# Optimization experiments

Measured on AMD Instinct MI355X. Metric: run time of the kernel, lower is better.

## Reference

```python
import jax, jax.numpy as jnp
import numpy as np

B, H, W, C = 8, 64, 64, 256  # N = H*W = 4096, pooled length N//2 = 2048


def setup_inputs() -> dict:
    key = jax.random.key(0)
    k1, k2, k3, k4 = jax.random.split(key, 4)
    scale = np.sqrt(2.0 / C).astype(np.float32)  # he_normal for 1x1 conv
    return {
        "x": jax.random.normal(k1, (B, H, W, C), dtype=jnp.float32),
        "w_theta": jax.random.normal(k2, (C, C), dtype=jnp.float32) * scale,
        "w_phi": jax.random.normal(k3, (C, C), dtype=jnp.float32) * scale,
        "w_g": jax.random.normal(k4, (C, C), dtype=jnp.float32) * scale,
    }


def _maxpool1d(z):
    # MaxPool1D(pool_size=2, strides=2, padding='valid') over axis 1
    b, n, c = z.shape
    return jnp.max(z.reshape(b, n // 2, 2, c), axis=2)


def reference(x, w_theta, w_phi, w_g):
    b, h, w, c = x.shape
    n = h * w
    xf = x.reshape(b, n, c)                       # [B, N, C]
    theta = xf @ w_theta                          # [B, N, C] (1x1 conv)
    phi = _maxpool1d(xf @ w_phi)                  # [B, N//2, C]
    f = jnp.einsum('bnc,bmc->bnm', theta, phi)    # [B, N, N//2] affinity
    f = jax.nn.softmax(f, axis=-1)
    g = _maxpool1d(xf @ w_g)                      # [B, N//2, C]
    y = jnp.einsum('bnm,bmc->bnc', f, g)          # [B, N, C]
    y = y.reshape(b, h, w, c)
    return x + y                                  # residual
```

## Files before the change

kernel.cpp:

```cpp
#include <hip/hip_runtime.h>
#include <stdint.h>

#define CC 256
#define NN 4096
#define MM 2048
#define BB 8
#define NROWS (BB*NN)
#define PROWS (BB*MM)

typedef __attribute__((ext_vector_type(8))) short    short8;
typedef __attribute__((ext_vector_type(8))) _Float16 half8;
typedef __attribute__((ext_vector_type(4))) float    float4v;

__device__ __forceinline__ unsigned short f2bf(float f) {
    unsigned int u = __float_as_uint(f);
    u += 0x7fffu + ((u >> 16) & 1u);
    return (unsigned short)(u >> 16);
}
__device__ __forceinline__ float bf2f(unsigned short h) {
    return __uint_as_float(((unsigned int)h) << 16);
}
__device__ __forceinline__ unsigned short f2h(float f) {
    union { _Float16 h; unsigned short u; } cv; cv.h = (_Float16)f; return cv.u;
}
__device__ __forceinline__ float h2f(unsigned short u) {
    union { _Float16 h; unsigned short u; } cv; cv.u = u; return (float)cv.h;
}

__global__ __launch_bounds__(256) void xsplit_kernel(
    const float* __restrict__ x,
    unsigned short* __restrict__ x_hi,
    unsigned short* __restrict__ x_lo)
{
    const size_t i = ((size_t)blockIdx.x*256 + threadIdx.x) * 8;
    float4v a0 = *(const float4v*)(x + i);
    float4v a1 = *(const float4v*)(x + i + 4);
    short8 h, l;
    #pragma unroll
    for (int j = 0; j < 4; ++j) {
        unsigned short h0 = f2bf(a0[j]);
        h[j]   = (short)h0; l[j]   = (short)f2bf(a0[j] - bf2f(h0));
        unsigned short h1 = f2bf(a1[j]);
        h[4+j] = (short)h1; l[4+j] = (short)f2bf(a1[j] - bf2f(h1));
    }
    *(short8*)(x_hi + i) = h;
    *(short8*)(x_lo + i) = l;
}

__global__ void wsplit_kernel(const float* __restrict__ w_theta,
                              const float* __restrict__ w_phi,
                              const float* __restrict__ w_g,
                              unsigned short* __restrict__ wT_hi,
                              unsigned short* __restrict__ wT_lo)
{
    __shared__ float tile[64][65];
    const int widx = blockIdx.z;
    const int kt = blockIdx.x, ct = blockIdx.y;
    const float* w = (widx == 0) ? w_theta : (widx == 1) ? w_phi : w_g;
    const int t  = threadIdx.x;
    const int tc = t & 63, tr = t >> 6;
    #pragma unroll
    for (int i = 0; i < 16; ++i) {
        const int lk = tr*16 + i;
        tile[lk][tc] = w[(size_t)(kt*64 + lk)*CC + ct*64 + tc];
    }
    __syncthreads();
    #pragma unroll
    for (int i = 0; i < 16; ++i) {
        const int lc = tr*16 + i;
        float v = tile[tc][lc];
        const int c = ct*64 + lc, k = kt*64 + tc;
        unsigned short hh = f2bf(v);
        size_t o = ((size_t)widx*CC + c)*CC + k;
        wT_hi[o] = hh;
        wT_lo[o] = f2bf(v - bf2f(hh));
    }
}

__global__ __launch_bounds__(256, 4) void proj_kernel(
    const unsigned short* __restrict__ x_hi,
    const unsigned short* __restrict__ x_lo,
    const unsigned short* __restrict__ wT_hi,
    const unsigned short* __restrict__ wT_lo,
    unsigned short* __restrict__ th,
    unsigned short* __restrict__ ph,
    unsigned short* __restrict__ g_f)
{
    __shared__ unsigned short wt_hi[64*136];
    __shared__ unsigned short wt_lo[64*136];

    const int tid  = threadIdx.x;
    const int rb   = blockIdx.x & 511;
    const int cv   = blockIdx.x >> 9;
    const int r0   = rb * 64;
    const int widx = cv >> 2;
    const int wc0  = (cv & 3) * 64;
    const unsigned short* wThp = wT_hi + ((size_t)widx*CC + wc0)*CC;
    const unsigned short* wTlp = wT_lo + ((size_t)widx*CC + wc0)*CC;
    const bool split3 = (widx < 2);

    const int wv   = tid >> 6;
    const int lane = tid & 63;
    const int quad = lane >> 4;
    const int l15  = lane & 15;
    const int arow = r0 + wv*16 + l15;
    const unsigned short* axh = x_hi + (size_t)arow*CC + quad*8;
    const unsigned short* axl = x_lo + (size_t)arow*CC + quad*8;

    float4v acc[4];
    #pragma unroll
    for (int nf = 0; nf < 4; ++nf) acc[nf] = (float4v){0.f,0.f,0.f,0.f};

    for (int h = 0; h < 2; ++h) {
        __syncthreads();
        {
            const int j    = tid & 63;
            const int kseg = tid >> 6;
            const size_t base = (size_t)j*CC + h*128 + kseg*32;
            const unsigned short* sh = wThp + base;
            unsigned short* dh = &wt_hi[j*136 + kseg*32];
            #pragma unroll
            for (int u = 0; u < 4; ++u)
                *(uint4*)(dh + u*8) = *(const uint4*)(sh + u*8);
            if (split3) {
                const unsigned short* sl = wTlp + base;
                unsigned short* dl = &wt_lo[j*136 + kseg*32];
                #pragma unroll
                for (int u = 0; u < 4; ++u)
                    *(uint4*)(dl + u*8) = *(const uint4*)(sl + u*8);
            }
        }
        __syncthreads();

        #pragma unroll
        for (int ks = 0; ks < 4; ++ks) {
            short8 a_hi = *(const short8*)(axh + h*128 + ks*32);
            short8 a_lo;
            if (split3) a_lo = *(const short8*)(axl + h*128 + ks*32);
            #pragma unroll
            for (int nf = 0; nf < 4; ++nf) {
                const int wrow = nf*16 + l15;
                short8 b_hi = *(const short8*)&wt_hi[wrow*136 + ks*32 + quad*8];
                acc[nf] = __builtin_amdgcn_mfma_f32_16x16x32_bf16(a_hi, b_hi, acc[nf], 0,0,0);
                if (split3) {
                    short8 b_lo = *(const short8*)&wt_lo[wrow*136 + ks*32 + quad*8];
                    acc[nf] = __builtin_amdgcn_mfma_f32_16x16x32_bf16(a_hi, b_lo, acc[nf], 0,0,0);
                    acc[nf] = __builtin_amdgcn_mfma_f32_16x16x32_bf16(a_lo, b_hi, acc[nf], 0,0,0);
                }
            }
        }
    }

    const int rowbase = r0 + wv*16 + quad*4;
    if (widx == 0) {
        #pragma unroll
        for (int nf = 0; nf < 4; ++nf) {
            const int c = wc0 + nf*16 + l15;
            #pragma unroll
            for (int r = 0; r < 4; ++r)
                th[(size_t)(rowbase + r)*CC + c] = f2h(acc[nf][r]);
        }
    } else if (widx == 1) {
        #pragma unroll
        for (int nf = 0; nf < 4; ++nf) {
            const int c = wc0 + nf*16 + l15;
            #pragma unroll
            for (int rp = 0; rp < 2; ++rp) {
                float v = fmaxf(acc[nf][2*rp], acc[nf][2*rp+1]);
                const int prow = rowbase/2 + rp;
                ph[(size_t)prow*CC + c] = f2h(v);
            }
        }
    } else {
        #pragma unroll
        for (int nf = 0; nf < 4; ++nf) {
            const int c = wc0 + nf*16 + l15;
            const int ct = c >> 4;
            const int c15 = c & 15;
            #pragma unroll
            for (int rp = 0; rp < 2; ++rp) {
                float v = fmaxf(acc[nf][2*rp], acc[nf][2*rp+1]);
                const int prow = rowbase/2 + rp;
                const int b  = prow >> 11;
                const int m  = prow & 2047;
                const int kt = m >> 5;
                const int km = m & 31;
                const int lane_t = (km >> 3)*16 + c15;
                const int j = km & 7;
                g_f[(((size_t)(b*64 + kt)*16 + ct)*64 + lane_t)*8 + j] = f2bf(v);
            }
        }
    }
}

__global__ void phimean_kernel(const unsigned short* __restrict__ ph,
                               float* __restrict__ phbar)
{
    const int b = blockIdx.x >> 6, chunk = blockIdx.x & 63;
    const int c = threadIdx.x;
    const size_t base = ((size_t)b*MM + chunk*32)*CC + c;
    float s = 0.f;
    for (int r = 0; r < 32; ++r) s += h2f(ph[base + (size_t)r*CC]);
    atomicAdd(&phbar[b*CC + c], s * (1.0f/MM));
}

__global__ __launch_bounds__(256, 3) void attn_kernel(
    const float* __restrict__ x,
    const unsigned short* __restrict__ th,
    const unsigned short* __restrict__ ph,
    const unsigned short* __restrict__ g_f,
    const float* __restrict__ phbar,
    float* __restrict__ out)
{
    __shared__ unsigned short s_ph[2][32*264];
    __shared__ unsigned short s_p[4][16*40];
    __shared__ float          s_l[64];

    const int tid  = threadIdx.x;
    const int bb   = blockIdx.x & 7;
    const int qt   = blockIdx.x >> 3;
    const int q0   = bb*NN + qt*64;
    const int b    = bb;
    const int wv   = tid >> 6;
    const int lane = tid & 63;
    const int quad = lane >> 4;
    const int l15  = lane & 15;

    const int sti = tid >> 3;
    const int stc = (tid & 7) * 32;
    const size_t phbase = (size_t)b * MM * CC;
    const unsigned short* stsrc = ph + phbase + (size_t)sti*CC + stc;

    half8 t_hi[8];
    {
        const unsigned short* bh = th + (size_t)(q0 + wv*16 + l15)*CC;
        #pragma unroll
        for (int ks = 0; ks < 8; ++ks)
            t_hi[ks] = *(const half8*)(bh + ks*32 + quad*8);
    }

    float sh128[4];
    {
        float sp = 0.f;
        #pragma unroll
        for (int ks = 0; ks < 8; ++ks) {
            const int k0 = ks*32 + quad*8;
            float4v m0 = *(const float4v*)&phbar[b*CC + k0];
            float4v m1 = *(const float4v*)&phbar[b*CC + k0 + 4];
            #pragma unroll
            for (int j = 0; j < 4; ++j) {
                sp += (float)t_hi[ks][j]   * m0[j];
                sp += (float)t_hi[ks][4+j] * m1[j];
            }
        }
        sp += __shfl_xor(sp, 16);
        sp += __shfl_xor(sp, 32);
        #pragma unroll
        for (int r = 0; r < 4; ++r)
            sh128[r] = __shfl(sp, quad*4 + r) + 128.f;
    }

    float4v O[4][4];
    #pragma unroll
    for (int rt = 0; rt < 4; ++rt)
        #pragma unroll
        for (int ct = 0; ct < 4; ++ct) O[rt][ct] = (float4v){0.f,0.f,0.f,0.f};
    float4v accl = (float4v){0.f,0.f,0.f,0.f};

    short8 ones;
    #pragma unroll
    for (int j = 0; j < 8; ++j) ones[j] = (short)0x3F80;

    const unsigned short* glf = g_f + (size_t)b*MM*CC + (size_t)lane*8;

    {
        unsigned short* dh = &s_ph[0][sti*264 + stc];
        #pragma unroll
        for (int u = 0; u < 4; ++u)
            *(uint4*)(dh + u*8) = *(const uint4*)(stsrc + u*8);
    }
    __syncthreads();

    for (int kt = 0; kt < 64; ++kt) {
        const int key0 = kt * 32;
        const int cur  = kt & 1;

        uint4 stg[4];
        if (kt < 63) {
            const unsigned short* sn = stsrc + (size_t)(key0 + 32)*CC;
            #pragma unroll
            for (int u = 0; u < 4; ++u) stg[u] = *(const uint4*)(sn + u*8);
        }
        short8 gf[4];
        #pragma unroll
        for (int ct = 0; ct < 4; ++ct)
            gf[ct] = *(const short8*)(glf + (size_t)(kt*16 + wv*4 + ct)*512);

        float4v S0 = (float4v){0.f,0.f,0.f,0.f};
        float4v S1 = (float4v){0.f,0.f,0.f,0.f};
        #pragma unroll
        for (int ks = 0; ks < 8; ++ks) {
            half8 b0 = *(const half8*)&s_ph[cur][( 0 + l15)*264 + ks*32 + quad*8];
            half8 b1 = *(const half8*)&s_ph[cur][(16 + l15)*264 + ks*32 + quad*8];
            S0 = __builtin_amdgcn_mfma_f32_16x16x32_f16(t_hi[ks], b0, S0, 0,0,0);
            S1 = __builtin_amdgcn_mfma_f32_16x16x32_f16(t_hi[ks], b1, S1, 0,0,0);
        }

        unsigned short* pw = &s_p[wv][0];
        #pragma unroll
        for (int r = 0; r < 4; ++r) {
            float a0 = fminf(fmaxf(S0[r] - sh128[r], -85.f), 85.f);
            float a1 = fminf(fmaxf(S1[r] - sh128[r], -85.f), 85.f);
            pw[(quad*4 + r)*40 + l15]      = f2bf(__expf(a0));
            pw[(quad*4 + r)*40 + 16 + l15] = f2bf(__expf(a1));
        }
        asm volatile("s_waitcnt lgkmcnt(0)" ::: "memory");
        short8 pown = *(const short8*)&s_p[wv][l15*40 + quad*8];
        accl = __builtin_amdgcn_mfma_f32_16x16x32_bf16(pown, ones, accl, 0,0,0);

        if (kt < 63) {
            unsigned short* dh = &s_ph[cur ^ 1][sti*264 + stc];
            #pragma unroll
            for (int u = 0; u < 4; ++u) *(uint4*)(dh + u*8) = stg[u];
        }
        __syncthreads();

        #pragma unroll
        for (int rt = 0; rt < 4; ++rt) {
            short8 pA = *(const short8*)&s_p[rt][l15*40 + quad*8];
            #pragma unroll
            for (int ct = 0; ct < 4; ++ct)
                O[rt][ct] = __builtin_amdgcn_mfma_f32_16x16x32_bf16(pA, gf[ct], O[rt][ct], 0,0,0);
        }
        __syncthreads();
    }

    if (l15 == 0) {
        #pragma unroll
        for (int r = 0; r < 4; ++r) s_l[wv*16 + quad*4 + r] = accl[r];
    }
    __syncthreads();

    #pragma unroll
    for (int rt = 0; rt < 4; ++rt) {
        #pragma unroll
        for (int r = 0; r < 4; ++r) {
            const int row = q0 + rt*16 + quad*4 + r;
            const float rl = 1.0f / s_l[rt*16 + quad*4 + r];
            #pragma unroll
            for (int ct = 0; ct < 4; ++ct) {
                const int c = wv*64 + ct*16 + l15;
                const size_t idx = (size_t)row*CC + c;
                out[idx] = x[idx] + O[rt][ct][r] * rl;
            }
        }
    }
}

extern "C" void kernel_launch(void* const* d_in, const int* in_sizes, int n_in,
                              void* d_out, int out_size, void* d_ws, size_t ws_size,
                              hipStream_t stream) {
    const float* x       = (const float*)d_in[0];
    const float* w_theta = (const float*)d_in[1];
    const float* w_phi   = (const float*)d_in[2];
    const float* w_g     = (const float*)d_in[3];
    float* out = (float*)d_out;

    unsigned short* th    = (unsigned short*)d_ws;
    unsigned short* ph    = th    + (size_t)NROWS*CC;
    unsigned short* g_f   = ph    + (size_t)PROWS*CC;
    unsigned short* x_hi  = g_f   + (size_t)PROWS*CC;
    unsigned short* x_lo  = x_hi  + (size_t)NROWS*CC;
    unsigned short* wT_hi = x_lo  + (size_t)NROWS*CC;
    unsigned short* wT_lo = wT_hi + (size_t)3*CC*CC;
    float*          phbar = (float*)(wT_lo + (size_t)3*CC*CC);

    hipMemsetAsync(phbar, 0, BB*CC*sizeof(float), stream);
    xsplit_kernel<<<NROWS*CC/8/256, 256, 0, stream>>>(x, x_hi, x_lo);
    wsplit_kernel<<<dim3(4,4,3), 256, 0, stream>>>(w_theta, w_phi, w_g, wT_hi, wT_lo);
    proj_kernel<<<6144, 256, 0, stream>>>(x_hi, x_lo, wT_hi, wT_lo, th, ph, g_f);
    phimean_kernel<<<512, 256, 0, stream>>>(ph, phbar);
    attn_kernel<<<NROWS/64, 256, 0, stream>>>(x, th, ph, g_f, phbar, out);
}
```

Before: 270.8 us.

## Store phi in MFMA fragment layout and read it directly from global memory

The projection kernel now writes pooled phi in a layout pre-arranged to match the MFMA B-fragment order. The attention kernel then loads phi fragments straight from global memory (cache) per wave, dropping the double-buffered LDS staging of phi. The phimean kernel is adapted to the new layout. This removes LDS traffic and the staging loads/stores, but every wave now issues its own global loads for the same phi tile, raising cache traffic and exposing load latency without explicit prefetch.

Result: slower. 302.7 us (+11.8%).

```diff
diff --git a/kernel.cpp b/kernel.cpp
--- a/kernel.cpp
+++ b/kernel.cpp
@@ -163,12 +163,19 @@
     } else if (widx == 1) {
         #pragma unroll
         for (int nf = 0; nf < 4; ++nf) {
-            const int c = wc0 + nf*16 + l15;
+            const int c  = wc0 + nf*16 + l15;
+            const int ks = c >> 5;
+            const int qd = (c >> 3) & 3;
+            const int j  = c & 7;
             #pragma unroll
             for (int rp = 0; rp < 2; ++rp) {
                 float v = fmaxf(acc[nf][2*rp], acc[nf][2*rp+1]);
                 const int prow = rowbase/2 + rp;
-                ph[(size_t)prow*CC + c] = f2h(v);
+                const int bq  = prow >> 11;
+                const int m   = prow & 2047;
+                const int kg  = m >> 4;
+                const int l15k = m & 15;
+                ph[((size_t)(bq*128 + kg)*8 + ks)*512 + (qd*16 + l15k)*8 + j] = f2h(v);
             }
         }
     } else {
@@ -198,9 +205,16 @@
 {
     const int b = blockIdx.x >> 6, chunk = blockIdx.x & 63;
     const int c = threadIdx.x;
-    const size_t base = ((size_t)b*MM + chunk*32)*CC + c;
+    const int ks = c >> 5, qd = (c >> 3) & 3, j = c & 7;
     float s = 0.f;
-    for (int r = 0; r < 32; ++r) s += h2f(ph[base + (size_t)r*CC]);
+    #pragma unroll
+    for (int kk = 0; kk < 2; ++kk) {
+        const int kg = chunk*2 + kk;
+        const unsigned short* base =
+            ph + ((size_t)(b*128 + kg)*8 + ks)*512 + qd*128 + j;
+        #pragma unroll
+        for (int l = 0; l < 16; ++l) s += h2f(base[l*8]);
+    }
     atomicAdd(&phbar[b*CC + c], s * (1.0f/MM));
 }
 
@@ -212,7 +226,6 @@
     const float* __restrict__ phbar,
     float* __restrict__ out)
 {
-    __shared__ unsigned short s_ph[2][32*264];
     __shared__ unsigned short s_p[4][16*40];
     __shared__ float          s_l[64];
 
@@ -226,11 +239,6 @@
     const int quad = lane >> 4;
     const int l15  = lane & 15;
 
-    const int sti = tid >> 3;
-    const int stc = (tid & 7) * 32;
-    const size_t phbase = (size_t)b * MM * CC;
-    const unsigned short* stsrc = ph + phbase + (size_t)sti*CC + stc;
-
     half8 t_hi[8];
     {
         const unsigned short* bh = th + (size_t)(q0 + wv*16 + l15)*CC;
@@ -272,25 +280,11 @@
     for (int j = 0; j < 8; ++j) ones[j] = (short)0x3F80;
 
     const unsigned short* glf = g_f + (size_t)b*MM*CC + (size_t)lane*8;
-
-    {
-        unsigned short* dh = &s_ph[0][sti*264 + stc];
-        #pragma unroll
-        for (int u = 0; u < 4; ++u)
-            *(uint4*)(dh + u*8) = *(const uint4*)(stsrc + u*8);
-    }
-    __syncthreads();
+    const unsigned short* phf = ph  + (size_t)b*MM*CC + (size_t)lane*8;
 
     for (int kt = 0; kt < 64; ++kt) {
-        const int key0 = kt * 32;
-        const int cur  = kt & 1;
-
-        uint4 stg[4];
-        if (kt < 63) {
-            const unsigned short* sn = stsrc + (size_t)(key0 + 32)*CC;
-            #pragma unroll
-            for (int u = 0; u < 4; ++u) stg[u] = *(const uint4*)(sn + u*8);
-        }
+        const int cur = kt & 1;  (void)cur;
+
         short8 gf[4];
         #pragma unroll
         for (int ct = 0; ct < 4; ++ct)
@@ -300,8 +294,8 @@
         float4v S1 = (float4v){0.f,0.f,0.f,0.f};
         #pragma unroll
         for (int ks = 0; ks < 8; ++ks) {
-            half8 b0 = *(const half8*)&s_ph[cur][( 0 + l15)*264 + ks*32 + quad*8];
-            half8 b1 = *(const half8*)&s_ph[cur][(16 + l15)*264 + ks*32 + quad*8];
+            half8 b0 = *(const half8*)(phf + (size_t)((kt*2 + 0)*8 + ks)*512);
+            half8 b1 = *(const half8*)(phf + (size_t)((kt*2 + 1)*8 + ks)*512);
             S0 = __builtin_amdgcn_mfma_f32_16x16x32_f16(t_hi[ks], b0, S0, 0,0,0);
             S1 = __builtin_amdgcn_mfma_f32_16x16x32_f16(t_hi[ks], b1, S1, 0,0,0);
         }
@@ -318,11 +312,6 @@
         short8 pown = *(const short8*)&s_p[wv][l15*40 + quad*8];
         accl = __builtin_amdgcn_mfma_f32_16x16x32_bf16(pown, ones, accl, 0,0,0);
 
-        if (kt < 63) {
-            unsigned short* dh = &s_ph[cur ^ 1][sti*264 + stc];
-            #pragma unroll
-            for (int u = 0; u < 4; ++u) *(uint4*)(dh + u*8) = stg[u];
-        }
         __syncthreads();
 
         #pragma unroll
```
